# Performance work log

Measured on AMD Instinct MI355X. Metric: run time of the kernel, lower is better.

Reference implementation:

```python
import jax, jax.numpy as jnp
import numpy as np

LEAKY = 0.2
BN_EPS = 1e-5
N_NODES = 50000
IN_F = 128
HID = 64
HEADS = 2
N_EDGES = 1600000


def _bn(x, gamma, beta):
    # BatchNorm1d in training mode: batch statistics over the node dim
    mu = jnp.mean(x, axis=0)
    var = jnp.mean((x - mu) ** 2, axis=0)
    return (x - mu) * jax.lax.rsqrt(var + BN_EPS) * gamma + beta


def _gat(x, src, dst, W, a_src, a_dst, bias, n):
    # W: [F_in, H*F], a_src/a_dst: [H, F]
    H, F = a_src.shape
    h = (x @ W).reshape(n, H, F)                      # [N,H,F]
    es = jnp.einsum('nhf,hf->nh', h, a_src)           # [N,H]
    ed = jnp.einsum('nhf,hf->nh', h, a_dst)           # [N,H]
    e = jax.nn.leaky_relu(es[src] + ed[dst], LEAKY)   # [E,H]
    m = jax.ops.segment_max(e, dst, num_segments=n)   # stable softmax per dst
    p = jnp.exp(e - m[dst])
    s = jax.ops.segment_sum(p, dst, num_segments=n)
    alpha = p / s[dst]                                # [E,H]
    out = jax.ops.segment_sum(h[src] * alpha[:, :, None], dst, num_segments=n)
    return out.reshape(n, H * F) + bias


def setup_inputs() -> dict:
    key = jax.random.key(0)
    ks = jax.random.split(key, 32)
    HF = HID * HEADS  # 128

    def g(k, shape, scale=0.1):
        return jax.random.normal(k, shape, dtype=jnp.float32) * scale

    inp = {
        'x': jax.random.normal(ks[0], (N_NODES, IN_F), dtype=jnp.float32),
        'edge_index': jax.random.randint(ks[1], (2, N_EDGES), 0, N_NODES, dtype=jnp.int64),
        # layer 1
        'W1': g(ks[2], (IN_F, HF)), 'as1': g(ks[3], (HEADS, HID)), 'ad1': g(ks[4], (HEADS, HID)),
        'gb1': jnp.zeros((HF,), jnp.float32),
        'lw1': g(ks[5], (IN_F, HF)), 'lb1': jnp.zeros((HF,), jnp.float32),
        'bg1': jnp.ones((IN_F,), jnp.float32), 'bb1': jnp.zeros((IN_F,), jnp.float32),
        # layer 2
        'W2': g(ks[6], (HF, HF)), 'as2': g(ks[7], (HEADS, HID)), 'ad2': g(ks[8], (HEADS, HID)),
        'gb2': jnp.zeros((HF,), jnp.float32),
        'lw2': g(ks[9], (HF, HF)), 'lb2': jnp.zeros((HF,), jnp.float32),
        'bg2': jnp.ones((HF,), jnp.float32), 'bb2': jnp.zeros((HF,), jnp.float32),
        # layer 3 (heads=1, out=2)
        'W3': g(ks[10], (HF, 2)), 'as3': g(ks[11], (1, 2)), 'ad3': g(ks[12], (1, 2)),
        'gb3': jnp.zeros((2,), jnp.float32),
        'lw3': g(ks[13], (HF, 2)), 'lb3': jnp.zeros((2,), jnp.float32),
        'bg3': jnp.ones((HF,), jnp.float32), 'bb3': jnp.zeros((HF,), jnp.float32),
    }
    return inp


def reference(x, edge_index,
              W1, as1, ad1, gb1, lw1, lb1, bg1, bb1,
              W2, as2, ad2, gb2, lw2, lb2, bg2, bb2,
              W3, as3, ad3, gb3, lw3, lb3, bg3, bb3):
    n = x.shape[0]
    loop = jnp.arange(n, dtype=edge_index.dtype)  # self-loops (PyG GAT default)
    src = jnp.concatenate([edge_index[0], loop])
    dst = jnp.concatenate([edge_index[1], loop])

    h = _bn(x, bg1, bb1)
    h = jax.nn.relu(h @ lw1 + lb1 + _gat(h, src, dst, W1, as1, ad1, gb1, n))
    h = _bn(h, bg2, bb2)
    h = jax.nn.relu(h @ lw2 + lb2 + _gat(h, src, dst, W2, as2, ad2, gb2, n))
    h = _bn(h, bg3, bb3)
    h = jax.nn.relu(h @ lw3 + lb3 + _gat(h, src, dst, W3, as3, ad3, gb3, n))
    return h
```

## Files before the change

### kernel.cpp

```cpp
#include <hip/hip_runtime.h>

#define LEAKY 0.2f
#define BN_EPS 1e-5f
#define BCHUNK 8192

typedef __bf16 v8bf __attribute__((ext_vector_type(8)));
typedef float v16f __attribute__((ext_vector_type(16)));
typedef float v2f __attribute__((ext_vector_type(2)));

__device__ __forceinline__ float wsum(float v) {
#pragma unroll
  for (int o = 32; o > 0; o >>= 1) v += __shfl_xor(v, o, 64);
  return v;
}

__device__ __forceinline__ float blo(unsigned u) { return __uint_as_float(u << 16); }
__device__ __forceinline__ float bhi(unsigned u) { return __uint_as_float(u & 0xffff0000u); }
__device__ __forceinline__ v2f bpair(unsigned u) {
  v2f r; r.x = __uint_as_float(u << 16); r.y = __uint_as_float(u & 0xffff0000u); return r;
}
__device__ __forceinline__ unsigned pack_bf16(float a, float b) {
  unsigned ua = __float_as_uint(a), ub = __float_as_uint(b);
  ua = (ua + 0x7fffu + ((ua >> 16) & 1u)) >> 16;
  ub = (ub + 0x7fffu + ((ub >> 16) & 1u)) >> 16;
  return ua | (ub << 16);
}
__device__ __forceinline__ unsigned short bf16of(float a) {
  unsigned ua = __float_as_uint(a);
  return (unsigned short)((ua + 0x7fffu + ((ua >> 16) & 1u)) >> 16);
}

__device__ __forceinline__ int edge_at(const void* ei, int is64, long long i) {
  return is64 ? (int)((const long long*)ei)[i] : ((const int*)ei)[i];
}

__global__ __launch_bounds__(256) void k_binA(const void* ei, int N, int E, int M,
                                              int nb, int nblk, int* counts) {
  __shared__ int hist[1024];
  __shared__ int sflag;
  int tid = threadIdx.x;
  if (tid < 64) {
    const long long* p = (const long long*)ei;
    long long v = p[tid];
    int bad = (v < 0 || v >= (long long)N) ? 1 : 0;
    unsigned long long mres = __ballot(bad);
    if (tid == 0) sflag = (mres == 0ull) ? 1 : 0;
  }
  for (int j = tid; j < nb; j += 256) hist[j] = 0;
  __syncthreads();
  int is64 = sflag;
  long long base = (long long)blockIdx.x * BCHUNK;
  int cnt = (int)min((long long)BCHUNK, (long long)M - base);
  for (int i = tid; i < cnt; i += 256) {
    long long g = base + i;
    int d = (g < E) ? edge_at(ei, is64, (long long)E + g) : (int)(g - E);
    atomicAdd(&hist[d >> 8], 1);
  }
  __syncthreads();
  for (int j = tid; j < nb; j += 256) counts[(size_t)j * nblk + blockIdx.x] = hist[j];
}

__global__ __launch_bounds__(1024) void k_binScan(int* counts, int total_entries) {
  __shared__ int part[1024];
  int tid = threadIdx.x;
  int per = (total_entries + 1023) / 1024;
  int lo = tid * per;
  int hi = lo + per; if (hi > total_entries) hi = total_entries;
  int s = 0;
  int i = lo;
  for (; i + 8 <= hi; i += 8) {
    int c0 = counts[i], c1 = counts[i + 1], c2 = counts[i + 2], c3 = counts[i + 3];
    int c4 = counts[i + 4], c5 = counts[i + 5], c6 = counts[i + 6], c7 = counts[i + 7];
    s += ((c0 + c1) + (c2 + c3)) + ((c4 + c5) + (c6 + c7));
  }
  for (; i < hi; ++i) s += counts[i];
  part[tid] = s;
  __syncthreads();
  for (int off = 1; off < 1024; off <<= 1) {
    int add = (tid >= off) ? part[tid - off] : 0;
    __syncthreads();
    part[tid] += add;
    __syncthreads();
  }
  int run = (tid == 0) ? 0 : part[tid - 1];
  i = lo;
  for (; i + 8 <= hi; i += 8) {
    int c0 = counts[i], c1 = counts[i + 1], c2 = counts[i + 2], c3 = counts[i + 3];
    int c4 = counts[i + 4], c5 = counts[i + 5], c6 = counts[i + 6], c7 = counts[i + 7];
    counts[i] = run; run += c0;
    counts[i + 1] = run; run += c1;
    counts[i + 2] = run; run += c2;
    counts[i + 3] = run; run += c3;
    counts[i + 4] = run; run += c4;
    counts[i + 5] = run; run += c5;
    counts[i + 6] = run; run += c6;
    counts[i + 7] = run; run += c7;
  }
  for (; i < hi; ++i) {
    int c = counts[i];
    counts[i] = run;
    run += c;
  }
}

__global__ __launch_bounds__(256) void k_binC(const void* ei, int N, int E, int M,
                                              int nb, int nblk, const int* counts, unsigned* tmp) {
  __shared__ int cur[1024];
  __shared__ int sflag;
  int tid = threadIdx.x;
  if (tid < 64) {
    const long long* p = (const long long*)ei;
    long long v = p[tid];
    int bad = (v < 0 || v >= (long long)N) ? 1 : 0;
    unsigned long long mres = __ballot(bad);
    if (tid == 0) sflag = (mres == 0ull) ? 1 : 0;
  }
  for (int j = tid; j < nb; j += 256) cur[j] = counts[(size_t)j * nblk + blockIdx.x];
  __syncthreads();
  int is64 = sflag;
  long long base = (long long)blockIdx.x * BCHUNK;
  int cnt = (int)min((long long)BCHUNK, (long long)M - base);
  for (int i = tid; i < cnt; i += 256) {
    long long g = base + i;
    int s, d;
    if (g < E) { s = edge_at(ei, is64, g); d = edge_at(ei, is64, (long long)E + g); }
    else       { s = d = (int)(g - E); }
    int pos = atomicAdd(&cur[d >> 8], 1);
    tmp[pos] = ((unsigned)s << 8) | (unsigned)(d & 255);
  }
}

__global__ __launch_bounds__(256) void k_binD(const unsigned* __restrict__ tmp,
                                              const int* __restrict__ counts,
                                              int nb, int nblk, int M, int N,
                                              int* __restrict__ rowptr, int* __restrict__ col) {
  __shared__ int scn[256];
  __shared__ int cur[256];
  int tid = threadIdx.x;
  int j = blockIdx.x;
  int base = counts[(size_t)j * nblk];
  int endv = (j + 1 < nb) ? counts[(size_t)(j + 1) * nblk] : M;
  int bc = endv - base;
  scn[tid] = 0;
  __syncthreads();
  for (int i = tid; i < bc; i += 256) atomicAdd(&scn[tmp[base + i] & 255], 1);
  __syncthreads();
  int v = scn[tid];
  __syncthreads();
  scn[tid] = v;
  __syncthreads();
  for (int off = 1; off < 256; off <<= 1) {
    int add = (tid >= off) ? scn[tid - off] : 0;
    __syncthreads();
    scn[tid] += add;
    __syncthreads();
  }
  int excl = scn[tid] - v;
  int d = (j << 8) + tid;
  if (d < N) rowptr[d] = base + excl;
  cur[tid] = base + excl;
  __syncthreads();
  for (int i = tid; i < bc; i += 256) {
    unsigned w = tmp[base + i];
    int pos = atomicAdd(&cur[w & 255], 1);
    col[pos] = (int)(w >> 8);
  }
  if (j == nb - 1 && tid == 0) rowptr[N] = M;
}

__global__ __launch_bounds__(128) void k_bnstats(const unsigned* __restrict__ xp,
                                                 int N, float* sums) {
  int f = threadIdx.x;
  int q = f >> 1, hi = f & 1;
  float s = 0.f, s2 = 0.f;
  for (int r = blockIdx.x; r < N; r += gridDim.x) {
    unsigned u = xp[(size_t)r * 64 + q];
    float v = hi ? bhi(u) : blo(u);
    s += v; s2 += v * v;
  }
  float* rep = sums + (size_t)(blockIdx.x & 7) * 256;
  atomicAdd(&rep[f], s);
  atomicAdd(&rep[128 + f], s2);
}

__global__ __launch_bounds__(256) void k_prep(
    const float* __restrict__ W1, const float* __restrict__ LW1,
    const float* __restrict__ W2, const float* __restrict__ LW2,
    const float* __restrict__ as1, const float* __restrict__ ad1,
    const float* __restrict__ as2, const float* __restrict__ ad2,
    const float* __restrict__ x, int N,
    unsigned short* __restrict__ Bp1, unsigned short* __restrict__ Bp2,
    float* __restrict__ stats1) {
  int blk = blockIdx.x;
  int tid = threadIdx.x;
  if (blk >= 34) {
    int b = blk - 34;
    int f = tid & 127;
    int half = tid >> 7;
    float s = 0.f, s2 = 0.f;
    for (int r = b + half * 1024; r < N; r += 2048) {
      float v = x[(size_t)r * 128 + f];
      s += v; s2 += v * v;
    }
    float* rep = stats1 + (size_t)(b & 7) * 256;
    atomicAdd(&rep[f], s);
    atomicAdd(&rep[128 + f], s2);
    return;
  }
  if (blk >= 32) {
    __shared__ float wes[128][4];
    const float* W = (blk == 32) ? W1 : W2;
    const float* as_ = (blk == 32) ? as1 : as2;
    const float* ad_ = (blk == 32) ? ad1 : ad2;
    unsigned short* Bp = (blk == 32) ? Bp1 : Bp2;
#pragma unroll
    for (int it = 0; it < 2; ++it) {
      int k = tid & 127;
      int c = (tid >> 7) + 2 * it;
      const float* a = (c < 2) ? as_ : ad_;
      int hb2 = (c & 1) * 64;
      float sum = 0.f;
      for (int f = 0; f < 64; ++f) sum += W[k * 128 + hb2 + f] * a[hb2 + f];
      wes[k][c] = sum;
    }
    __syncthreads();
    for (int fr = tid; fr < 512; fr += 256) {
      int lane = fr & 63, s = fr >> 6;
      int n = lane & 31;
      int k0 = s * 16 + (lane >> 5) * 8;
      unsigned short tb[8];
#pragma unroll
      for (int j = 0; j < 8; ++j)
        tb[j] = bf16of((n < 4) ? wes[k0 + j][n] : 0.f);
      uint4 pk;
      pk.x = (unsigned)tb[0] | ((unsigned)tb[1] << 16);
      pk.y = (unsigned)tb[2] | ((unsigned)tb[3] << 16);
      pk.z = (unsigned)tb[4] | ((unsigned)tb[5] << 16);
      pk.w = (unsigned)tb[6] | ((unsigned)tb[7] << 16);
      int fi = (64 + s) * 64 + lane;
      *(uint4*)&Bp[(size_t)fi * 8] = pk;
    }
    return;
  }
  const float* W  = (blk < 16) ? W1 : W2;
  const float* LW = (blk < 16) ? LW1 : LW2;
  unsigned short* Bp = (blk < 16) ? Bp1 : Bp2;
  int fi = (blk & 15) * 256 + tid;
  int lane = fi & 63, s = (fi >> 6) & 7, t = fi >> 9;
  int n = t * 32 + (lane & 31);
  int k0 = s * 16 + (lane >> 5) * 8;
  unsigned short tb[8];
#pragma unroll
  for (int j = 0; j < 8; ++j) {
    int k = k0 + j;
    float v = (n < 128) ? W[k * 128 + n] : LW[k * 128 + (n - 128)];
    tb[j] = bf16of(v);
  }
  uint4 pk;
  pk.x = (unsigned)tb[0] | ((unsigned)tb[1] << 16);
  pk.y = (unsigned)tb[2] | ((unsigned)tb[3] << 16);
  pk.z = (unsigned)tb[4] | ((unsigned)tb[5] << 16);
  pk.w = (unsigned)tb[6] | ((unsigned)tb[7] << 16);
  *(uint4*)&Bp[(size_t)fi * 8] = pk;
}

__global__ __launch_bounds__(256) void k_mm(
    const void* __restrict__ xin, int packed,
    const float* __restrict__ stats, const float* __restrict__ gamma, const float* __restrict__ beta,
    const unsigned short* __restrict__ Bp,
    unsigned* __restrict__ hb, unsigned* __restrict__ linp,
    float* __restrict__ es, float* __restrict__ ed, int N) {
  __shared__ __align__(16) unsigned short Al[32 * 136];
  __shared__ float scl_s[128], sht_s[128];
  int tid = threadIdx.x;
  int lane = tid & 63;
  int w = tid >> 6;
  int rowBase = blockIdx.x * 32;

  if (tid < 128) {
    float s = 0.f, s2 = 0.f;
#pragma unroll
    for (int r = 0; r < 8; ++r) {
      s += stats[r * 256 + tid];
      s2 += stats[r * 256 + 128 + tid];
    }
    float inv_n = 1.0f / (float)N;
    float mu = s * inv_n;
    float var = s2 * inv_n - mu * mu;
    float rs = rsqrtf(var + BN_EPS);
    float sc = gamma[tid] * rs;
    scl_s[tid] = sc;
    sht_s[tid] = beta[tid] - mu * sc;
  }

  v8bf bfrag[2][8];
#pragma unroll
  for (int t = 0; t < 2; ++t)
#pragma unroll
    for (int s = 0; s < 8; ++s) {
      int fi = ((2 * w + t) * 8 + s) * 64 + lane;
      bfrag[t][s] = *(const v8bf*)&Bp[(size_t)fi * 8];
    }
  __syncthreads();

  if (!packed) {
    const float* x = (const float*)xin;
    for (int q = tid; q < 32 * 32; q += 256) {
      int r = q >> 5, k4 = (q & 31) * 4;
      int row = rowBase + r;
      float4 v = make_float4(0.f, 0.f, 0.f, 0.f);
      if (row < N) v = *(const float4*)&x[(size_t)row * 128 + k4];
      unsigned p0 = pack_bf16(v.x * scl_s[k4] + sht_s[k4], v.y * scl_s[k4 + 1] + sht_s[k4 + 1]);
      unsigned p1 = pack_bf16(v.z * scl_s[k4 + 2] + sht_s[k4 + 2], v.w * scl_s[k4 + 3] + sht_s[k4 + 3]);
      *(uint2*)&Al[r * 136 + k4] = make_uint2(p0, p1);
    }
  } else {
    const unsigned* xp = (const unsigned*)xin;
    for (int q = tid; q < 32 * 16; q += 256) {
      int r = q >> 4, g = q & 15;
      int row = rowBase + r;
      uint4 u = make_uint4(0u, 0u, 0u, 0u);
      if (row < N) u = *(const uint4*)&xp[(size_t)row * 64 + g * 4];
      int f = g * 8;
      uint4 o;
      o.x = pack_bf16(blo(u.x) * scl_s[f] + sht_s[f], bhi(u.x) * scl_s[f + 1] + sht_s[f + 1]);
      o.y = pack_bf16(blo(u.y) * scl_s[f + 2] + sht_s[f + 2], bhi(u.y) * scl_s[f + 3] + sht_s[f + 3]);
      o.z = pack_bf16(blo(u.z) * scl_s[f + 4] + sht_s[f + 4], bhi(u.z) * scl_s[f + 5] + sht_s[f + 5]);
      o.w = pack_bf16(blo(u.w) * scl_s[f + 6] + sht_s[f + 6], bhi(u.w) * scl_s[f + 7] + sht_s[f + 7]);
      *(uint4*)&Al[r * 136 + f] = o;
    }
  }
  __syncthreads();

  int m = lane & 31, half = lane >> 5;
  v8bf afrag[8];
#pragma unroll
  for (int s = 0; s < 8; ++s)
    afrag[s] = *(const v8bf*)&Al[m * 136 + s * 16 + half * 8];

  v16f acc0 = {}, acc1 = {};
#pragma unroll
  for (int s = 0; s < 8; ++s) {
    acc0 = __builtin_amdgcn_mfma_f32_32x32x16_bf16(afrag[s], bfrag[0][s], acc0, 0, 0, 0);
    acc1 = __builtin_amdgcn_mfma_f32_32x32x16_bf16(afrag[s], bfrag[1][s], acc1, 0, 0, 0);
  }

  v16f acc2 = {};
  if (w == 0) {
#pragma unroll
    for (int s = 0; s < 8; ++s) {
      v8bf besf = *(const v8bf*)&Bp[(size_t)((64 + s) * 64 + lane) * 8];
      acc2 = __builtin_amdgcn_mfma_f32_32x32x16_bf16(afrag[s], besf, acc2, 0, 0, 0);
    }
  }

  int mlo = half * 4;
  int t0 = 2 * w, t1 = 2 * w + 1;
#pragma unroll
  for (int r = 0; r < 16; ++r) {
    int row = (r & 3) + 8 * (r >> 2) + mlo;
    int node = rowBase + row;
    float a0 = acc0[r], a1 = acc1[r];
    float b0 = __shfl_xor(a0, 1, 64);
    float b1 = __shfl_xor(a1, 1, 64);
    if (node < N && !(lane & 1)) {
      if (t0 < 4) {
        hb[(size_t)node * 64 + (t0 * 16 + (m >> 1))] = pack_bf16(a0, b0);
        hb[(size_t)node * 64 + (t1 * 16 + (m >> 1))] = pack_bf16(a1, b1);
      } else {
        linp[(size_t)node * 64 + ((t0 - 4) * 16 + (m >> 1))] = pack_bf16(a0, b0);
        linp[(size_t)node * 64 + ((t1 - 4) * 16 + (m >> 1))] = pack_bf16(a1, b1);
      }
    }
    if (w == 0 && m < 4 && node < N) {
      float v = acc2[r];
      if (m < 2) es[2 * node + (m & 1)] = v;
      else       ed[2 * node + (m & 1)] = v;
    }
  }
}

__global__ __launch_bounds__(256) void k_agg(
    const int* __restrict__ rowptr, const int* __restrict__ col,
    const float* __restrict__ es, const float* __restrict__ ed,
    const unsigned* __restrict__ hb, const unsigned* __restrict__ linp,
    const float* __restrict__ lb, const float* __restrict__ gb,
    unsigned* __restrict__ xoutp, int N) {
  int lane = threadIdx.x & 63;
  int w = threadIdx.x >> 6;
  int d = blockIdx.x * 4 + w;
  if (d >= N) return;
  int start = rowptr[d], end = rowptr[d + 1];
  v2f edv = *(const v2f*)&ed[2 * d];
  int q = lane >> 4;
  int m = lane & 15;
  int head_hi = m >= 8;
  v2f zero = {0.f, 0.f};
  v2f lk = {LEAKY, LEAKY};

  v2f acc[4] = {zero, zero, zero, zero};
  v2f sp = zero;
  int i = start;
  for (; i + 16 <= end; i += 16) {
#pragma unroll
    for (int b = 0; b < 4; ++b) {
      int idx = i + 4 * b + q;
      int s = col[idx];
      v2f ev = *(const v2f*)&es[2 * s];
      uint4 u = *(const uint4*)&hb[(size_t)s * 64 + m * 4];
      v2f e = ev + edv;
      v2f le = __builtin_elementwise_max(e, zero) + lk * __builtin_elementwise_min(e, zero);
      v2f p; p.x = __expf(le.x); p.y = __expf(le.y);
      sp += p;
      float f = head_hi ? p.y : p.x;
      v2f fv = {f, f};
      acc[0] = __builtin_elementwise_fma(fv, bpair(u.x), acc[0]);
      acc[1] = __builtin_elementwise_fma(fv, bpair(u.y), acc[1]);
      acc[2] = __builtin_elementwise_fma(fv, bpair(u.z), acc[2]);
      acc[3] = __builtin_elementwise_fma(fv, bpair(u.w), acc[3]);
    }
  }
  for (; i < end; i += 4) {
    int idx = i + q;
    int valid = idx < end;
    int s = col[valid ? idx : end - 1];
    v2f ev = *(const v2f*)&es[2 * s];
    uint4 u = *(const uint4*)&hb[(size_t)s * 64 + m * 4];
    v2f e = ev + edv;
    v2f le = __builtin_elementwise_max(e, zero) + lk * __builtin_elementwise_min(e, zero);
    v2f p; p.x = __expf(le.x); p.y = __expf(le.y);
    if (!valid) p = zero;
    sp += p;
    float f = head_hi ? p.y : p.x;
    v2f fv = {f, f};
    acc[0] = __builtin_elementwise_fma(fv, bpair(u.x), acc[0]);
    acc[1] = __builtin_elementwise_fma(fv, bpair(u.y), acc[1]);
    acc[2] = __builtin_elementwise_fma(fv, bpair(u.z), acc[2]);
    acc[3] = __builtin_elementwise_fma(fv, bpair(u.w), acc[3]);
  }
#pragma unroll
  for (int k = 0; k < 4; ++k) {
    acc[k].x += __shfl_xor(acc[k].x, 16, 64);
    acc[k].x += __shfl_xor(acc[k].x, 32, 64);
    acc[k].y += __shfl_xor(acc[k].y, 16, 64);
    acc[k].y += __shfl_xor(acc[k].y, 32, 64);
  }
  sp.x += __shfl_xor(sp.x, 16, 64); sp.x += __shfl_xor(sp.x, 32, 64);
  sp.y += __shfl_xor(sp.y, 16, 64); sp.y += __shfl_xor(sp.y, 32, 64);

  if (q == 0) {
    float inv = 1.0f / (head_hi ? sp.y : sp.x);
    uint4 lv = *(const uint4*)&linp[(size_t)d * 64 + m * 4];
    int f8 = 8 * m;
    float4 lb0 = *(const float4*)&lb[f8], lb1 = *(const float4*)&lb[f8 + 4];
    float4 gb0 = *(const float4*)&gb[f8], gb1 = *(const float4*)&gb[f8 + 4];
    float v0 = blo(lv.x) + lb0.x + acc[0].x * inv + gb0.x;
    float v1 = bhi(lv.x) + lb0.y + acc[0].y * inv + gb0.y;
    float v2 = blo(lv.y) + lb0.z + acc[1].x * inv + gb0.z;
    float v3 = bhi(lv.y) + lb0.w + acc[1].y * inv + gb0.w;
    float v4 = blo(lv.z) + lb1.x + acc[2].x * inv + gb1.x;
    float v5 = bhi(lv.z) + lb1.y + acc[2].y * inv + gb1.y;
    float v6 = blo(lv.w) + lb1.z + acc[3].x * inv + gb1.z;
    float v7 = bhi(lv.w) + lb1.w + acc[3].y * inv + gb1.w;
    v0 = v0 > 0.f ? v0 : 0.f; v1 = v1 > 0.f ? v1 : 0.f;
    v2 = v2 > 0.f ? v2 : 0.f; v3 = v3 > 0.f ? v3 : 0.f;
    v4 = v4 > 0.f ? v4 : 0.f; v5 = v5 > 0.f ? v5 : 0.f;
    v6 = v6 > 0.f ? v6 : 0.f; v7 = v7 > 0.f ? v7 : 0.f;
    uint4 o;
    o.x = pack_bf16(v0, v1); o.y = pack_bf16(v2, v3);
    o.z = pack_bf16(v4, v5); o.w = pack_bf16(v6, v7);
    *(uint4*)&xoutp[(size_t)d * 64 + m * 4] = o;
  }
}

__global__ __launch_bounds__(256) void k_l3node(
    const unsigned* __restrict__ xp,
    const float* __restrict__ stats, const float* __restrict__ gamma, const float* __restrict__ beta,
    const float* __restrict__ W3, const float* __restrict__ LW3,
    const float* __restrict__ as3, const float* __restrict__ ad3,
    float* h3, float* lin3, float* es3, float* ed3, int N) {
  int lane = threadIdx.x & 63;
  int n = blockIdx.x * 4 + (threadIdx.x >> 6);
  if (n >= N) return;
  float inv_n = 1.0f / (float)N;
  int f0 = lane, f1 = 64 + lane;
  float su0 = 0.f, sq0 = 0.f, su1 = 0.f, sq1 = 0.f;
#pragma unroll
  for (int r = 0; r < 8; ++r) {
    su0 += stats[r * 256 + f0];  sq0 += stats[r * 256 + 128 + f0];
    su1 += stats[r * 256 + f1];  sq1 += stats[r * 256 + 128 + f1];
  }
  float mu0 = su0 * inv_n;
  float var0 = sq0 * inv_n - mu0 * mu0;
  float rs0 = rsqrtf(var0 + BN_EPS);
  float sc0 = gamma[f0] * rs0, sh0 = beta[f0] - mu0 * sc0;
  float mu1 = su1 * inv_n;
  float var1 = sq1 * inv_n - mu1 * mu1;
  float rs1 = rsqrtf(var1 + BN_EPS);
  float sc1 = gamma[f1] * rs1, sh1 = beta[f1] - mu1 * sc1;

  unsigned ua = xp[(size_t)n * 64 + (lane >> 1)];
  unsigned ub = xp[(size_t)n * 64 + 32 + (lane >> 1)];
  float xv0 = (lane & 1) ? bhi(ua) : blo(ua);
  float xv1 = (lane & 1) ? bhi(ub) : blo(ub);
  float xn0 = xv0 * sc0 + sh0;
  float xn1 = xv1 * sc1 + sh1;

  float2 w0 = *(const float2*)&W3[lane * 2];
  float2 w1 = *(const float2*)&W3[(64 + lane) * 2];
  float2 l0 = *(const float2*)&LW3[lane * 2];
  float2 l1 = *(const float2*)&LW3[(64 + lane) * 2];
  float hc0 = wsum(xn0 * w0.x + xn1 * w1.x);
  float hc1 = wsum(xn0 * w0.y + xn1 * w1.y);
  float lc0 = wsum(xn0 * l0.x + xn1 * l1.x);
  float lc1 = wsum(xn0 * l0.y + xn1 * l1.y);
  if (lane == 0) {
    h3[2 * n] = hc0; h3[2 * n + 1] = hc1;
    lin3[2 * n] = lc0; lin3[2 * n + 1] = lc1;
    es3[n] = hc0 * as3[0] + hc1 * as3[1];
    ed3[n] = hc0 * ad3[0] + hc1 * ad3[1];
  }
}

__global__ __launch_bounds__(256) void k_agg3(
    const int* __restrict__ rowptr, const int* __restrict__ col,
    const float* __restrict__ es, const float* __restrict__ ed,
    const float* __restrict__ h3, const float* __restrict__ lin3,
    const float* __restrict__ lb3, const float* __restrict__ gb3,
    float* __restrict__ out, int N) {
  int lane = threadIdx.x & 63;
  int d = blockIdx.x * 4 + (threadIdx.x >> 6);
  if (d >= N) return;
  int start = rowptr[d], end = rowptr[d + 1];
  float edd = ed[d];
  float ps = 0.f, a0 = 0.f, a1 = 0.f;
  for (int i = start + lane; i < end; i += 64) {
    int s = col[i];
    float e = es[s] + edd; e = e > 0.f ? e : LEAKY * e;
    float p = __expf(e);
    float2 hv = *(const float2*)&h3[2 * s];
    ps += p; a0 += p * hv.x; a1 += p * hv.y;
  }
  ps = wsum(ps); a0 = wsum(a0); a1 = wsum(a1);
  if (lane < 2) {
    float a = (lane == 0 ? a0 : a1) / ps;
    float v = lin3[2 * d + lane] + lb3[lane] + a + gb3[lane];
    out[2 * d + lane] = v > 0.f ? v : 0.f;
  }
}

extern "C" void kernel_launch(void* const* d_in, const int* in_sizes, int n_in,
                              void* d_out, int out_size, void* d_ws, size_t ws_size,
                              hipStream_t stream) {
  const float* x   = (const float*)d_in[0];
  const void*  ei  = d_in[1];
  const float* W1  = (const float*)d_in[2];
  const float* as1 = (const float*)d_in[3];
  const float* ad1 = (const float*)d_in[4];
  const float* gb1 = (const float*)d_in[5];
  const float* lw1 = (const float*)d_in[6];
  const float* lb1 = (const float*)d_in[7];
  const float* bg1 = (const float*)d_in[8];
  const float* bb1 = (const float*)d_in[9];
  const float* W2  = (const float*)d_in[10];
  const float* as2 = (const float*)d_in[11];
  const float* ad2 = (const float*)d_in[12];
  const float* gb2 = (const float*)d_in[13];
  const float* lw2 = (const float*)d_in[14];
  const float* lb2 = (const float*)d_in[15];
  const float* bg2 = (const float*)d_in[16];
  const float* bb2 = (const float*)d_in[17];
  const float* W3  = (const float*)d_in[18];
  const float* as3 = (const float*)d_in[19];
  const float* ad3 = (const float*)d_in[20];
  const float* gb3 = (const float*)d_in[21];
  const float* lw3 = (const float*)d_in[22];
  const float* lb3 = (const float*)d_in[23];
  const float* bg3 = (const float*)d_in[24];
  const float* bb3 = (const float*)d_in[25];
  float* out = (float*)d_out;

  int N = in_sizes[0] / 128;
  int E = in_sizes[1] / 2;
  int M = E + N;
  int nb = (N + 255) >> 8;
  int nblk = (M + BCHUNK - 1) / BCHUNK;

  char* wsp = (char*)d_ws;
  size_t off = 0;
  auto alloc = [&](size_t bytes) -> void* {
    void* p = wsp + off;
    off = (off + bytes + 255) & ~(size_t)255;
    return p;
  };
  int* rowptr   = (int*)alloc(((size_t)N + 1) * 4);
  int* col      = (int*)alloc((size_t)M * 4);
  unsigned* tmp = (unsigned*)alloc((size_t)M * 4);
  int* counts   = (int*)alloc(((size_t)nb * nblk + 1) * 4);
  float* st1    = (float*)alloc(8 * 256 * 4);
  float* st2    = (float*)alloc(8 * 256 * 4);
  float* st3    = (float*)alloc(8 * 256 * 4);
  unsigned short* Bp1 = (unsigned short*)alloc(4608 * 16);
  unsigned short* Bp2 = (unsigned short*)alloc(4608 * 16);
  unsigned* hbp  = (unsigned*)alloc((size_t)N * 64 * 4);
  unsigned* linp = (unsigned*)alloc((size_t)N * 64 * 4);
  unsigned* x2p  = (unsigned*)alloc((size_t)N * 64 * 4);
  float* es    = (float*)alloc((size_t)N * 2 * 4);
  float* edb   = (float*)alloc((size_t)N * 2 * 4);
  float* h3    = (float*)alloc((size_t)N * 2 * 4);
  float* lin3  = (float*)alloc((size_t)N * 2 * 4);
  float* es3   = (float*)alloc((size_t)N * 4);
  float* ed3   = (float*)alloc((size_t)N * 4);
  (void)ws_size; (void)n_in; (void)out_size;

  hipMemsetAsync(st1, 0, 3 * 8 * 256 * 4, stream);

  k_binA<<<nblk, 256, 0, stream>>>(ei, N, E, M, nb, nblk, counts);
  k_binScan<<<1, 1024, 0, stream>>>(counts, nb * nblk);
  k_binC<<<nblk, 256, 0, stream>>>(ei, N, E, M, nb, nblk, counts, tmp);
  k_binD<<<nb, 256, 0, stream>>>(tmp, counts, nb, nblk, M, N, rowptr, col);

  k_prep<<<34 + 1024, 256, 0, stream>>>(W1, lw1, W2, lw2, as1, ad1, as2, ad2,
                                        x, N, Bp1, Bp2, st1);

  int gnode = (N + 3) / 4;
  int gmm = (N + 31) / 32;

  k_mm<<<gmm, 256, 0, stream>>>(x, 0, st1, bg1, bb1, Bp1, hbp, linp, es, edb, N);
  k_agg<<<gnode, 256, 0, stream>>>(rowptr, col, es, edb, hbp, linp, lb1, gb1, x2p, N);

  k_bnstats<<<1024, 128, 0, stream>>>(x2p, N, st2);
  k_mm<<<gmm, 256, 0, stream>>>(x2p, 1, st2, bg2, bb2, Bp2, hbp, linp, es, edb, N);
  k_agg<<<gnode, 256, 0, stream>>>(rowptr, col, es, edb, hbp, linp, lb2, gb2, x2p, N);

  k_bnstats<<<1024, 128, 0, stream>>>(x2p, N, st3);
  k_l3node<<<gnode, 256, 0, stream>>>(x2p, st3, bg3, bb3, W3, lw3, as3, ad3,
                                      h3, lin3, es3, ed3, N);
  k_agg3<<<gnode, 256, 0, stream>>>(rowptr, col, es3, ed3, h3, lin3, lb3, gb3, out, N);
}
```

Measured before the change: 441.8 us.

## Co-launch CSR binning with weight prep and first matmul, shrink bucket size

Merges the CSR-building histogram pass into the weight-prep/BN-stats kernel and the scatter pass into the layer-1 matmul kernel via block-index dispatch, so graph construction overlaps with independent dense work and two launches disappear. Bucket width is halved from 256 to 128 destinations, doubling bucket count and making the per-bucket local sort in binD cheaper with more parallel blocks. It trades a larger counts array for the scan and mixed-role blocks sharing one LDS allocation, which may affect occupancy.

```diff
diff --git a/kernel.cpp b/kernel.cpp
--- a/kernel.cpp
+++ b/kernel.cpp
@@ -34,248 +34,74 @@
   return is64 ? (int)((const long long*)ei)[i] : ((const int*)ei)[i];
 }
 
-__global__ __launch_bounds__(256) void k_binA(const void* ei, int N, int E, int M,
-                                              int nb, int nblk, int* counts) {
-  __shared__ int hist[1024];
-  __shared__ int sflag;
+
+__device__ __forceinline__ void binA_body(int blk, const void* ei, int N, int E, int M,
+                                          int nb, int nblk, int* counts, int* lds) {
+  int* hist = lds;
+  int* sflag = lds + 1024;
   int tid = threadIdx.x;
   if (tid < 64) {
     const long long* p = (const long long*)ei;
     long long v = p[tid];
     int bad = (v < 0 || v >= (long long)N) ? 1 : 0;
     unsigned long long mres = __ballot(bad);
-    if (tid == 0) sflag = (mres == 0ull) ? 1 : 0;
+    if (tid == 0) *sflag = (mres == 0ull) ? 1 : 0;
   }
   for (int j = tid; j < nb; j += 256) hist[j] = 0;
   __syncthreads();
-  int is64 = sflag;
-  long long base = (long long)blockIdx.x * BCHUNK;
+  int is64 = *sflag;
+  long long base = (long long)blk * BCHUNK;
   int cnt = (int)min((long long)BCHUNK, (long long)M - base);
   for (int i = tid; i < cnt; i += 256) {
     long long g = base + i;
     int d = (g < E) ? edge_at(ei, is64, (long long)E + g) : (int)(g - E);
-    atomicAdd(&hist[d >> 8], 1);
-  }
-  __syncthreads();
-  for (int j = tid; j < nb; j += 256) counts[(size_t)j * nblk + blockIdx.x] = hist[j];
-}
-
-__global__ __launch_bounds__(1024) void k_binScan(int* counts, int total_entries) {
-  __shared__ int part[1024];
-  int tid = threadIdx.x;
-  int per = (total_entries + 1023) / 1024;
-  int lo = tid * per;
-  int hi = lo + per; if (hi > total_entries) hi = total_entries;
-  int s = 0;
-  int i = lo;
-  for (; i + 8 <= hi; i += 8) {
-    int c0 = counts[i], c1 = counts[i + 1], c2 = counts[i + 2], c3 = counts[i + 3];
-    int c4 = counts[i + 4], c5 = counts[i + 5], c6 = counts[i + 6], c7 = counts[i + 7];
-    s += ((c0 + c1) + (c2 + c3)) + ((c4 + c5) + (c6 + c7));
-  }
-  for (; i < hi; ++i) s += counts[i];
-  part[tid] = s;
-  __syncthreads();
-  for (int off = 1; off < 1024; off <<= 1) {
-    int add = (tid >= off) ? part[tid - off] : 0;
-    __syncthreads();
-    part[tid] += add;
-    __syncthreads();
-  }
-  int run = (tid == 0) ? 0 : part[tid - 1];
-  i = lo;
-  for (; i + 8 <= hi; i += 8) {
-    int c0 = counts[i], c1 = counts[i + 1], c2 = counts[i + 2], c3 = counts[i + 3];
-    int c4 = counts[i + 4], c5 = counts[i + 5], c6 = counts[i + 6], c7 = counts[i + 7];
-    counts[i] = run; run += c0;
-    counts[i + 1] = run; run += c1;
-    counts[i + 2] = run; run += c2;
-    counts[i + 3] = run; run += c3;
-    counts[i + 4] = run; run += c4;
-    counts[i + 5] = run; run += c5;
-    counts[i + 6] = run; run += c6;
-    counts[i + 7] = run; run += c7;
-  }
-  for (; i < hi; ++i) {
-    int c = counts[i];
-    counts[i] = run;
-    run += c;
-  }
-}
-
-__global__ __launch_bounds__(256) void k_binC(const void* ei, int N, int E, int M,
-                                              int nb, int nblk, const int* counts, unsigned* tmp) {
-  __shared__ int cur[1024];
-  __shared__ int sflag;
+    atomicAdd(&hist[d >> 7], 1);
+  }
+  __syncthreads();
+  for (int j = tid; j < nb; j += 256) counts[(size_t)j * nblk + blk] = hist[j];
+}
+
+__device__ __forceinline__ void binC_body(int blk, const void* ei, int N, int E, int M,
+                                          int nb, int nblk, const int* counts,
+                                          unsigned* tmp, int* lds) {
+  int* cur = lds;
+  int* sflag = lds + 1024;
   int tid = threadIdx.x;
   if (tid < 64) {
     const long long* p = (const long long*)ei;
     long long v = p[tid];
     int bad = (v < 0 || v >= (long long)N) ? 1 : 0;
     unsigned long long mres = __ballot(bad);
-    if (tid == 0) sflag = (mres == 0ull) ? 1 : 0;
-  }
-  for (int j = tid; j < nb; j += 256) cur[j] = counts[(size_t)j * nblk + blockIdx.x];
-  __syncthreads();
-  int is64 = sflag;
-  long long base = (long long)blockIdx.x * BCHUNK;
+    if (tid == 0) *sflag = (mres == 0ull) ? 1 : 0;
+  }
+  for (int j = tid; j < nb; j += 256) cur[j] = counts[(size_t)j * nblk + blk];
+  __syncthreads();
+  int is64 = *sflag;
+  long long base = (long long)blk * BCHUNK;
   int cnt = (int)min((long long)BCHUNK, (long long)M - base);
   for (int i = tid; i < cnt; i += 256) {
     long long g = base + i;
     int s, d;
     if (g < E) { s = edge_at(ei, is64, g); d = edge_at(ei, is64, (long long)E + g); }
     else       { s = d = (int)(g - E); }
-    int pos = atomicAdd(&cur[d >> 8], 1);
-    tmp[pos] = ((unsigned)s << 8) | (unsigned)(d & 255);
-  }
-}
-
-__global__ __launch_bounds__(256) void k_binD(const unsigned* __restrict__ tmp,
-                                              const int* __restrict__ counts,
-                                              int nb, int nblk, int M, int N,
-                                              int* __restrict__ rowptr, int* __restrict__ col) {
-  __shared__ int scn[256];
-  __shared__ int cur[256];
-  int tid = threadIdx.x;
-  int j = blockIdx.x;
-  int base = counts[(size_t)j * nblk];
-  int endv = (j + 1 < nb) ? counts[(size_t)(j + 1) * nblk] : M;
-  int bc = endv - base;
-  scn[tid] = 0;
-  __syncthreads();
-  for (int i = tid; i < bc; i += 256) atomicAdd(&scn[tmp[base + i] & 255], 1);
-  __syncthreads();
-  int v = scn[tid];
-  __syncthreads();
-  scn[tid] = v;
-  __syncthreads();
-  for (int off = 1; off < 256; off <<= 1) {
-    int add = (tid >= off) ? scn[tid - off] : 0;
-    __syncthreads();
-    scn[tid] += add;
-    __syncthreads();
-  }
-  int excl = scn[tid] - v;
-  int d = (j << 8) + tid;
-  if (d < N) rowptr[d] = base + excl;
-  cur[tid] = base + excl;
-  __syncthreads();
-  for (int i = tid; i < bc; i += 256) {
-    unsigned w = tmp[base + i];
-    int pos = atomicAdd(&cur[w & 255], 1);
-    col[pos] = (int)(w >> 8);
-  }
-  if (j == nb - 1 && tid == 0) rowptr[N] = M;
-}
-
-__global__ __launch_bounds__(128) void k_bnstats(const unsigned* __restrict__ xp,
-                                                 int N, float* sums) {
-  int f = threadIdx.x;
-  int q = f >> 1, hi = f & 1;
-  float s = 0.f, s2 = 0.f;
-  for (int r = blockIdx.x; r < N; r += gridDim.x) {
-    unsigned u = xp[(size_t)r * 64 + q];
-    float v = hi ? bhi(u) : blo(u);
-    s += v; s2 += v * v;
-  }
-  float* rep = sums + (size_t)(blockIdx.x & 7) * 256;
-  atomicAdd(&rep[f], s);
-  atomicAdd(&rep[128 + f], s2);
-}
-
-__global__ __launch_bounds__(256) void k_prep(
-    const float* __restrict__ W1, const float* __restrict__ LW1,
-    const float* __restrict__ W2, const float* __restrict__ LW2,
-    const float* __restrict__ as1, const float* __restrict__ ad1,
-    const float* __restrict__ as2, const float* __restrict__ ad2,
-    const float* __restrict__ x, int N,
-    unsigned short* __restrict__ Bp1, unsigned short* __restrict__ Bp2,
-    float* __restrict__ stats1) {
-  int blk = blockIdx.x;
-  int tid = threadIdx.x;
-  if (blk >= 34) {
-    int b = blk - 34;
-    int f = tid & 127;
-    int half = tid >> 7;
-    float s = 0.f, s2 = 0.f;
-    for (int r = b + half * 1024; r < N; r += 2048) {
-      float v = x[(size_t)r * 128 + f];
-      s += v; s2 += v * v;
-    }
-    float* rep = stats1 + (size_t)(b & 7) * 256;
-    atomicAdd(&rep[f], s);
-    atomicAdd(&rep[128 + f], s2);
-    return;
-  }
-  if (blk >= 32) {
-    __shared__ float wes[128][4];
-    const float* W = (blk == 32) ? W1 : W2;
-    const float* as_ = (blk == 32) ? as1 : as2;
-    const float* ad_ = (blk == 32) ? ad1 : ad2;
-    unsigned short* Bp = (blk == 32) ? Bp1 : Bp2;
-#pragma unroll
-    for (int it = 0; it < 2; ++it) {
-      int k = tid & 127;
-      int c = (tid >> 7) + 2 * it;
-      const float* a = (c < 2) ? as_ : ad_;
-      int hb2 = (c & 1) * 64;
-      float sum = 0.f;
-      for (int f = 0; f < 64; ++f) sum += W[k * 128 + hb2 + f] * a[hb2 + f];
-      wes[k][c] = sum;
-    }
-    __syncthreads();
-    for (int fr = tid; fr < 512; fr += 256) {
-      int lane = fr & 63, s = fr >> 6;
-      int n = lane & 31;
-      int k0 = s * 16 + (lane >> 5) * 8;
-      unsigned short tb[8];
-#pragma unroll
-      for (int j = 0; j < 8; ++j)
-        tb[j] = bf16of((n < 4) ? wes[k0 + j][n] : 0.f);
-      uint4 pk;
-      pk.x = (unsigned)tb[0] | ((unsigned)tb[1] << 16);
-      pk.y = (unsigned)tb[2] | ((unsigned)tb[3] << 16);
-      pk.z = (unsigned)tb[4] | ((unsigned)tb[5] << 16);
-      pk.w = (unsigned)tb[6] | ((unsigned)tb[7] << 16);
-      int fi = (64 + s) * 64 + lane;
-      *(uint4*)&Bp[(size_t)fi * 8] = pk;
-    }
-    return;
-  }
-  const float* W  = (blk < 16) ? W1 : W2;
-  const float* LW = (blk < 16) ? LW1 : LW2;
-  unsigned short* Bp = (blk < 16) ? Bp1 : Bp2;
-  int fi = (blk & 15) * 256 + tid;
-  int lane = fi & 63, s = (fi >> 6) & 7, t = fi >> 9;
-  int n = t * 32 + (lane & 31);
-  int k0 = s * 16 + (lane >> 5) * 8;
-  unsigned short tb[8];
-#pragma unroll
-  for (int j = 0; j < 8; ++j) {
-    int k = k0 + j;
-    float v = (n < 128) ? W[k * 128 + n] : LW[k * 128 + (n - 128)];
-    tb[j] = bf16of(v);
-  }
-  uint4 pk;
-  pk.x = (unsigned)tb[0] | ((unsigned)tb[1] << 16);
-  pk.y = (unsigned)tb[2] | ((unsigned)tb[3] << 16);
-  pk.z = (unsigned)tb[4] | ((unsigned)tb[5] << 16);
-  pk.w = (unsigned)tb[6] | ((unsigned)tb[7] << 16);
-  *(uint4*)&Bp[(size_t)fi * 8] = pk;
-}
-
-__global__ __launch_bounds__(256) void k_mm(
-    const void* __restrict__ xin, int packed,
-    const float* __restrict__ stats, const float* __restrict__ gamma, const float* __restrict__ beta,
-    const unsigned short* __restrict__ Bp,
-    unsigned* __restrict__ hb, unsigned* __restrict__ linp,
-    float* __restrict__ es, float* __restrict__ ed, int N) {
-  __shared__ __align__(16) unsigned short Al[32 * 136];
-  __shared__ float scl_s[128], sht_s[128];
+    int pos = atomicAdd(&cur[d >> 7], 1);
+    tmp[pos] = ((unsigned)s << 7) | (unsigned)(d & 127);
+  }
+}
+
+#define MM_SMEM (32 * 136 * 2 + 128 * 4 + 128 * 4)
+
+__device__ __forceinline__ void mm_body(int blk, const void* xin, int packed,
+    const float* stats, const float* gamma, const float* beta,
+    const unsigned short* Bp, unsigned* hb, unsigned* linp,
+    float* es, float* ed, int N, char* smem) {
+  unsigned short* Al = (unsigned short*)smem;
+  float* scl_s = (float*)(smem + 8704);
+  float* sht_s = (float*)(smem + 8704 + 512);
   int tid = threadIdx.x;
   int lane = tid & 63;
   int w = tid >> 6;
-  int rowBase = blockIdx.x * 32;
+  int rowBase = blk * 32;
 
   if (tid < 128) {
     float s = 0.f, s2 = 0.f;
@@ -378,6 +204,213 @@
       else       ed[2 * node + (m & 1)] = v;
     }
   }
+}
+
+
+__global__ __launch_bounds__(256) void k_prepA(
+    const float* __restrict__ W1, const float* __restrict__ LW1,
+    const float* __restrict__ W2, const float* __restrict__ LW2,
+    const float* __restrict__ as1, const float* __restrict__ ad1,
+    const float* __restrict__ as2, const float* __restrict__ ad2,
+    const float* __restrict__ x, int N,
+    unsigned short* __restrict__ Bp1, unsigned short* __restrict__ Bp2,
+    float* __restrict__ stats1,
+    const void* ei, int E, int M, int nb, int nblk, int* counts) {
+  __shared__ __align__(16) int lds[1025];
+  int blk = blockIdx.x;
+  int tid = threadIdx.x;
+  if (blk >= 1058) { binA_body(blk - 1058, ei, N, E, M, nb, nblk, counts, lds); return; }
+  if (blk >= 34) {
+    int b = blk - 34;
+    int f = tid & 127;
+    int half = tid >> 7;
+    float s = 0.f, s2 = 0.f;
+    for (int r = b + half * 1024; r < N; r += 2048) {
+      float v = x[(size_t)r * 128 + f];
+      s += v; s2 += v * v;
+    }
+    float* rep = stats1 + (size_t)(b & 7) * 256;
+    atomicAdd(&rep[f], s);
+    atomicAdd(&rep[128 + f], s2);
+    return;
+  }
+  if (blk >= 32) {
+    float (*wes)[4] = (float(*)[4])lds;
+    const float* W = (blk == 32) ? W1 : W2;
+    const float* as_ = (blk == 32) ? as1 : as2;
+    const float* ad_ = (blk == 32) ? ad1 : ad2;
+    unsigned short* Bp = (blk == 32) ? Bp1 : Bp2;
+#pragma unroll
+    for (int it = 0; it < 2; ++it) {
+      int k = tid & 127;
+      int c = (tid >> 7) + 2 * it;
+      const float* a = (c < 2) ? as_ : ad_;
+      int hb2 = (c & 1) * 64;
+      float sum = 0.f;
+      for (int f = 0; f < 64; ++f) sum += W[k * 128 + hb2 + f] * a[hb2 + f];
+      wes[k][c] = sum;
+    }
+    __syncthreads();
+    for (int fr = tid; fr < 512; fr += 256) {
+      int lane = fr & 63, s = fr >> 6;
+      int n = lane & 31;
+      int k0 = s * 16 + (lane >> 5) * 8;
+      unsigned short tb[8];
+#pragma unroll
+      for (int j = 0; j < 8; ++j)
+        tb[j] = bf16of((n < 4) ? wes[k0 + j][n] : 0.f);
+      uint4 pk;
+      pk.x = (unsigned)tb[0] | ((unsigned)tb[1] << 16);
+      pk.y = (unsigned)tb[2] | ((unsigned)tb[3] << 16);
+      pk.z = (unsigned)tb[4] | ((unsigned)tb[5] << 16);
+      pk.w = (unsigned)tb[6] | ((unsigned)tb[7] << 16);
+      int fi = (64 + s) * 64 + lane;
+      *(uint4*)&Bp[(size_t)fi * 8] = pk;
+    }
+    return;
+  }
+  const float* W  = (blk < 16) ? W1 : W2;
+  const float* LW = (blk < 16) ? LW1 : LW2;
+  unsigned short* Bp = (blk < 16) ? Bp1 : Bp2;
+  int fi = (blk & 15) * 256 + tid;
+  int lane = fi & 63, s = (fi >> 6) & 7, t = fi >> 9;
+  int n = t * 32 + (lane & 31);
+  int k0 = s * 16 + (lane >> 5) * 8;
+  unsigned short tb[8];
+#pragma unroll
+  for (int j = 0; j < 8; ++j) {
+    int k = k0 + j;
+    float v = (n < 128) ? W[k * 128 + n] : LW[k * 128 + (n - 128)];
+    tb[j] = bf16of(v);
+  }
+  uint4 pk;
+  pk.x = (unsigned)tb[0] | ((unsigned)tb[1] << 16);
+  pk.y = (unsigned)tb[2] | ((unsigned)tb[3] << 16);
+  pk.z = (unsigned)tb[4] | ((unsigned)tb[5] << 16);
+  pk.w = (unsigned)tb[6] | ((unsigned)tb[7] << 16);
+  *(uint4*)&Bp[(size_t)fi * 8] = pk;
+}
+
+__global__ __launch_bounds__(1024) void k_binScan(int* counts, int total_entries) {
+  __shared__ int part[1024];
+  int tid = threadIdx.x;
+  int per = (total_entries + 1023) / 1024;
+  int lo = tid * per;
+  int hi = lo + per; if (hi > total_entries) hi = total_entries;
+  int s = 0;
+  int i = lo;
+  for (; i + 8 <= hi; i += 8) {
+    int c0 = counts[i], c1 = counts[i + 1], c2 = counts[i + 2], c3 = counts[i + 3];
+    int c4 = counts[i + 4], c5 = counts[i + 5], c6 = counts[i + 6], c7 = counts[i + 7];
+    s += ((c0 + c1) + (c2 + c3)) + ((c4 + c5) + (c6 + c7));
+  }
+  for (; i < hi; ++i) s += counts[i];
+  part[tid] = s;
+  __syncthreads();
+  for (int off = 1; off < 1024; off <<= 1) {
+    int add = (tid >= off) ? part[tid - off] : 0;
+    __syncthreads();
+    part[tid] += add;
+    __syncthreads();
+  }
+  int run = (tid == 0) ? 0 : part[tid - 1];
+  i = lo;
+  for (; i + 8 <= hi; i += 8) {
+    int c0 = counts[i], c1 = counts[i + 1], c2 = counts[i + 2], c3 = counts[i + 3];
+    int c4 = counts[i + 4], c5 = counts[i + 5], c6 = counts[i + 6], c7 = counts[i + 7];
+    counts[i] = run; run += c0;
+    counts[i + 1] = run; run += c1;
+    counts[i + 2] = run; run += c2;
+    counts[i + 3] = run; run += c3;
+    counts[i + 4] = run; run += c4;
+    counts[i + 5] = run; run += c5;
+    counts[i + 6] = run; run += c6;
+    counts[i + 7] = run; run += c7;
+  }
+  for (; i < hi; ++i) {
+    int c = counts[i];
+    counts[i] = run;
+    run += c;
+  }
+}
+
+__global__ __launch_bounds__(256) void k_mmC(
+    const void* __restrict__ xin, int packed,
+    const float* __restrict__ stats, const float* __restrict__ gamma, const float* __restrict__ beta,
+    const unsigned short* __restrict__ Bp,
+    unsigned* __restrict__ hb, unsigned* __restrict__ linp,
+    float* __restrict__ es, float* __restrict__ ed, int N, int gmm,
+    const void* ei, int E, int M, int nb, int nblk, const int* counts, unsigned* tmp) {
+  __shared__ __align__(16) char smem[MM_SMEM];
+  int blk = blockIdx.x;
+  if (blk < gmm) {
+    mm_body(blk, xin, packed, stats, gamma, beta, Bp, hb, linp, es, ed, N, smem);
+  } else {
+    binC_body(blk - gmm, ei, N, E, M, nb, nblk, counts, tmp, (int*)smem);
+  }
+}
+
+__global__ __launch_bounds__(256) void k_mm(
+    const void* __restrict__ xin, int packed,
+    const float* __restrict__ stats, const float* __restrict__ gamma, const float* __restrict__ beta,
+    const unsigned short* __restrict__ Bp,
+    unsigned* __restrict__ hb, unsigned* __restrict__ linp,
+    float* __restrict__ es, float* __restrict__ ed, int N) {
+  __shared__ __align__(16) char smem[MM_SMEM];
+  mm_body(blockIdx.x, xin, packed, stats, gamma, beta, Bp, hb, linp, es, ed, N, smem);
+}
+
+__global__ __launch_bounds__(256) void k_binD(const unsigned* __restrict__ tmp,
+                                              const int* __restrict__ counts,
+                                              int nb, int nblk, int M, int N,
+                                              int* __restrict__ rowptr, int* __restrict__ col) {
+  __shared__ int scn[128];
+  __shared__ int cur[128];
+  int tid = threadIdx.x;
+  int j = blockIdx.x;
+  int base = counts[(size_t)j * nblk];
+  int endv = (j + 1 < nb) ? counts[(size_t)(j + 1) * nblk] : M;
+  int bc = endv - base;
+  if (tid < 128) scn[tid] = 0;
+  __syncthreads();
+  for (int i = tid; i < bc; i += 256) atomicAdd(&scn[tmp[base + i] & 127], 1);
+  __syncthreads();
+  int v = (tid < 128) ? scn[tid] : 0;
+  __syncthreads();
+  for (int off = 1; off < 128; off <<= 1) {
+    int add = (tid >= off && tid < 128) ? scn[tid - off] : 0;
+    __syncthreads();
+    if (tid < 128) scn[tid] += add;
+    __syncthreads();
+  }
+  if (tid < 128) {
+    int excl = scn[tid] - v;
+    int d = (j << 7) + tid;
+    if (d < N) rowptr[d] = base + excl;
+    cur[tid] = base + excl;
+  }
+  __syncthreads();
+  for (int i = tid; i < bc; i += 256) {
+    unsigned w = tmp[base + i];
+    int pos = atomicAdd(&cur[w & 127], 1);
+    col[pos] = (int)(w >> 7);
+  }
+  if (j == nb - 1 && tid == 0) rowptr[N] = M;
+}
+
+__global__ __launch_bounds__(128) void k_bnstats(const unsigned* __restrict__ xp,
+                                                 int N, float* sums) {
+  int f = threadIdx.x;
+  int q = f >> 1, hi = f & 1;
+  float s = 0.f, s2 = 0.f;
+  for (int r = blockIdx.x; r < N; r += gridDim.x) {
+    unsigned u = xp[(size_t)r * 64 + q];
+    float v = hi ? bhi(u) : blo(u);
+    s += v; s2 += v * v;
+  }
+  float* rep = sums + (size_t)(blockIdx.x & 7) * 256;
+  atomicAdd(&rep[f], s);
+  atomicAdd(&rep[128 + f], s2);
 }
 
 __global__ __launch_bounds__(256) void k_agg(
@@ -583,7 +616,7 @@
   int N = in_sizes[0] / 128;
   int E = in_sizes[1] / 2;
   int M = E + N;
-  int nb = (N + 255) >> 8;
+  int nb = (N + 127) >> 7;
   int nblk = (M + BCHUNK - 1) / BCHUNK;
 
   char* wsp = (char*)d_ws;
@@ -615,18 +648,17 @@
 
   hipMemsetAsync(st1, 0, 3 * 8 * 256 * 4, stream);
 
-  k_binA<<<nblk, 256, 0, stream>>>(ei, N, E, M, nb, nblk, counts);
-  k_binScan<<<1, 1024, 0, stream>>>(counts, nb * nblk);
-  k_binC<<<nblk, 256, 0, stream>>>(ei, N, E, M, nb, nblk, counts, tmp);
-  k_binD<<<nb, 256, 0, stream>>>(tmp, counts, nb, nblk, M, N, rowptr, col);
-
-  k_prep<<<34 + 1024, 256, 0, stream>>>(W1, lw1, W2, lw2, as1, ad1, as2, ad2,
-                                        x, N, Bp1, Bp2, st1);
-
   int gnode = (N + 3) / 4;
   int gmm = (N + 31) / 32;
 
-  k_mm<<<gmm, 256, 0, stream>>>(x, 0, st1, bg1, bb1, Bp1, hbp, linp, es, edb, N);
+  k_prepA<<<1058 + nblk, 256, 0, stream>>>(W1, lw1, W2, lw2, as1, ad1, as2, ad2,
+                                           x, N, Bp1, Bp2, st1,
+                                           ei, E, M, nb, nblk, counts);
+  k_binScan<<<1, 1024, 0, stream>>>(counts, nb * nblk);
+  k_mmC<<<gmm + nblk, 256, 0, stream>>>(x, 0, st1, bg1, bb1, Bp1, hbp, linp, es, edb, N,
+                                        gmm, ei, E, M, nb, nblk, counts, tmp);
+  k_binD<<<nb, 256, 0, stream>>>(tmp, counts, nb, nblk, M, N, rowptr, col);
+
   k_agg<<<gnode, 256, 0, stream>>>(rowptr, col, es, edb, hbp, linp, lb1, gb1, x2p, N);
 
   k_bnstats<<<1024, 128, 0, stream>>>(x2p, N, st2);
```

New measurement: 433.6 us. About the same (-1.9%).
